# Kernel optimization log

Measured on AMD Instinct MI355X. Metric: run time of the kernel, lower is better.

The kernel has to match this reference:

```python
import jax, jax.numpy as jnp
import numpy as np

B, LATENT, HID, OUT, SEQ = 256, 512, 1024, 256, 128


def setup_inputs() -> dict:
    key = jax.random.key(0)
    ks = jax.random.split(key, 5)
    s = lambda fan: 1.0 / np.sqrt(fan)
    return {
        "latent": jax.random.normal(ks[0], (B, LATENT), jnp.float32),
        "fc_W": jax.random.normal(ks[1], (HID, LATENT), jnp.float32) * s(LATENT),
        "fc_b": jnp.zeros((HID,), jnp.float32),
        "W_ih": jax.random.normal(ks[2], (4 * HID, OUT), jnp.float32) * s(HID),
        "W_hh": jax.random.normal(ks[3], (4 * HID, HID), jnp.float32) * s(HID),
        "b_ih": jnp.zeros((4 * HID,), jnp.float32),
        "b_hh": jnp.zeros((4 * HID,), jnp.float32),
        "out_W": jax.random.normal(ks[4], (OUT, HID), jnp.float32) * s(HID),
        "out_b": jnp.zeros((OUT,), jnp.float32),
    }


def reference(latent, fc_W, fc_b, W_ih, W_hh, b_ih, b_hh, out_W, out_b):
    # hidden init from latent; cell init zero (num_layers = 1)
    h0 = latent @ fc_W.T + fc_b                       # [B, HID]
    c0 = jnp.zeros_like(h0)
    x0 = jnp.zeros((latent.shape[0], out_W.shape[0]), latent.dtype)  # [B, OUT]
    bias = b_ih + b_hh
    H = h0.shape[-1]

    def step(carry, _):
        x, h, c = carry
        gates = x @ W_ih.T + h @ W_hh.T + bias        # [B, 4H], torch order i,f,g,o
        i = jax.nn.sigmoid(gates[:, 0 * H:1 * H])
        f = jax.nn.sigmoid(gates[:, 1 * H:2 * H])
        g = jnp.tanh(gates[:, 2 * H:3 * H])
        o = jax.nn.sigmoid(gates[:, 3 * H:4 * H])
        c = f * c + i * g
        h = o * jnp.tanh(c)
        y = h @ out_W.T + out_b                        # [B, OUT]; fed back as next input
        return (y, h, c), y

    _, ys = jax.lax.scan(step, (x0, h0, c0), None, length=SEQ)
    return jnp.transpose(ys, (1, 0, 2))               # [B, SEQ, OUT]
```

## Files before the change

kernel.cpp:

```cpp
#include <hip/hip_runtime.h>


typedef __attribute__((ext_vector_type(8))) _Float16 f16x8;
typedef __attribute__((ext_vector_type(4))) float f32x4;
typedef __attribute__((ext_vector_type(4))) unsigned u32x4;

#define MFMA16(a,b,c) __builtin_amdgcn_mfma_f32_16x16x32_f16(a,b,c,0,0,0)

__device__ __forceinline__ short f2h(float x){
  return __builtin_bit_cast(short, (_Float16)x);
}
__device__ __forceinline__ unsigned pack2h(float a, float b){
  unsigned short ua = __builtin_bit_cast(unsigned short, (_Float16)a);
  unsigned short ub = __builtin_bit_cast(unsigned short, (_Float16)b);
  return (unsigned)ua | ((unsigned)ub << 16);
}

__device__ __forceinline__ void gll16(const void* g, void* l){
  __builtin_amdgcn_global_load_lds((const __attribute__((address_space(1))) void*)g,
                                   (__attribute__((address_space(3))) void*)l, 16, 0, 0);
}

__device__ __forceinline__ void vm0(){ asm volatile("s_waitcnt vmcnt(0)" ::: "memory"); }

__device__ __forceinline__ void stage_t(const short* gRC, int ldk, short* lds, int lane, int wv){
#pragma unroll
  for (int jj = 0; jj < 2; ++jj){
    int j = wv*2 + jj;
    const short* src = gRC + (size_t)(j*8 + (lane>>3))*ldk + ((lane&7)*8);
    gll16(src, lds + j*512);
  }
}

__device__ __forceinline__ f16x8 fragh(const short* t, int r, int kk, int lane){
  int row = r + (lane & 15);
  int k0  = (kk<<5) + ((lane>>4)<<3);
  return *(const f16x8*)(t + row*64 + (k0 ^ ((row & 7)<<3)));
}

template<int CH>
__device__ __forceinline__ void core_k(const short* Ag, const short* Bg, int ldk,
                                       short* As, short* Bs, f32x4 (&acc)[2][2],
                                       int lane, int wv, int wr, int wc){
  stage_t(Ag, ldk, As, lane, wv);
  stage_t(Bg, ldk, Bs, lane, wv);
  __syncthreads();
  int buf = 0;
  for (int c = 0; c < CH; ++c){
    if (c+1 < CH){
      stage_t(Ag + (c+1)*64, ldk, As + (buf^1)*4096, lane, wv);
      stage_t(Bg + (c+1)*64, ldk, Bs + (buf^1)*4096, lane, wv);
    }
    const short* At = As + buf*4096;
    const short* Bt = Bs + buf*4096;
#pragma unroll
    for (int kk = 0; kk < 2; ++kk){
      f16x8 a0 = fragh(At, wr,    kk, lane), a1 = fragh(At, wr+16, kk, lane);
      f16x8 b0 = fragh(Bt, wc,    kk, lane), b1 = fragh(Bt, wc+16, kk, lane);
      acc[0][0] = MFMA16(a0,b0,acc[0][0]); acc[0][1] = MFMA16(a0,b1,acc[0][1]);
      acc[1][0] = MFMA16(a1,b0,acc[1][0]); acc[1][1] = MFMA16(a1,b1,acc[1][1]);
    }
    __syncthreads();
    buf ^= 1;
  }
}


__global__ void k_prep(const float* __restrict__ W_ih, const float* __restrict__ out_W,
                       const float* __restrict__ latent, const float* __restrict__ fc_W,
                       const float* __restrict__ W_hh,
                       const float* __restrict__ b_ih, const float* __restrict__ b_hh,
                       short* __restrict__ WihF, short* __restrict__ owT,
                       short* __restrict__ owB, short* __restrict__ latF,
                       short* __restrict__ fcwF, short* __restrict__ W0F,
                       float* __restrict__ bias0, unsigned* __restrict__ flags){
  int T = blockDim.x*gridDim.x, t0 = blockIdx.x*blockDim.x + threadIdx.x;
  for (int i = t0; i < 8192; i += T) flags[i] = 0u;
  for (int idx = t0; idx < 4096*256; idx += T){
    int r = idx >> 8, j = idx & 255;
    WihF[(size_t)r*256 + (j ^ ((r&7)<<3))] = f2h(W_ih[idx]);
  }
  for (int idx = t0; idx < 1024*256; idx += T){
    int c = idx >> 8, j = idx & 255;
    owT[(size_t)c*256 + (j ^ ((c&7)<<3))] = f2h(out_W[(size_t)j*1024 + c]);
  }
  for (int idx = t0; idx < 256*1024; idx += T){
    int o = idx >> 10, k = idx & 1023;
    owB[(size_t)o*1024 + (k ^ ((o&7)<<3))] = f2h(out_W[idx]);
  }
  for (int idx = t0; idx < 256*512; idx += T){
    int b = idx >> 9, j = idx & 511;
    latF[(size_t)b*512 + (j ^ ((b&7)<<3))] = f2h(latent[idx]);
  }
  for (int idx = t0; idx < 1024*512; idx += T){
    int n = idx >> 9, j = idx & 511;
    fcwF[(size_t)n*512 + (j ^ ((n&7)<<3))] = f2h(fc_W[idx]);
  }
  for (int idx = t0; idx < 4096*1024; idx += T){
    int r = idx >> 10, k = idx & 1023;
    int p = ((r & 1023)<<2) | (r >> 10);
    size_t a = ((size_t)(p>>4)*32 + (k>>5))*512 + ((size_t)((((k>>3)&3)<<4)|(p&15)))*8 + (k&7);
    W0F[a] = f2h(W_hh[idx]);
  }
  for (int r = t0; r < 4096; r += T){
    int rp = ((r & 1023)<<2) | (r >> 10);
    bias0[rp] = b_ih[r] + b_hh[r];
  }
}

__global__ void k_bias1(const float* __restrict__ W_ih, const float* __restrict__ out_b,
                        const float* __restrict__ bias0, float* __restrict__ bias1){
  int r = blockIdx.x*256 + threadIdx.x;
  float s = 0.f;
  for (int j = 0; j < 256; ++j) s += W_ih[(size_t)r*256 + j]*out_b[j];
  int rp = ((r & 1023)<<2) | (r >> 10);
  bias1[rp] = bias0[rp] + s;
}

__global__ __launch_bounds__(256) void k_wtotal(const short* __restrict__ WihF,
                                                const short* __restrict__ owT,
                                                const float* __restrict__ W_hh,
                                                short* __restrict__ WtF){
  __shared__ __align__(16) short As[2*4096];
  __shared__ __align__(16) short Bs[2*4096];
  int tid = threadIdx.x, lane = tid & 63, wv = tid >> 6;
  int wr = (wv>>1)*32, wc = (wv&1)*32;
  int Rm = blockIdx.x*64, Rn = blockIdx.y*64;
  f32x4 acc[2][2] = {};
  core_k<4>(WihF + (size_t)Rm*256, owT + (size_t)Rn*256, 256, As, Bs, acc, lane, wv, wr, wc);
#pragma unroll
  for (int mi = 0; mi < 2; ++mi)
#pragma unroll
  for (int ni = 0; ni < 2; ++ni)
#pragma unroll
  for (int r = 0; r < 4; ++r){
    int row = Rm + wr + mi*16 + ((lane>>4)<<2) + r;
    int col = Rn + wc + ni*16 + (lane & 15);
    float v = acc[mi][ni][r] + W_hh[(size_t)row*1024 + col];
    int p = ((row & 1023)<<2) | (row >> 10);
    size_t a = ((size_t)(p>>4)*32 + (col>>5))*512 + ((size_t)((((col>>3)&3)<<4)|(p&15)))*8 + (col&7);
    WtF[a] = f2h(v);
  }
}

__global__ __launch_bounds__(256) void k_h0(const short* __restrict__ latF,
                                            const short* __restrict__ fcwF,
                                            const float* __restrict__ fc_b,
                                            short* __restrict__ A0){
  __shared__ __align__(16) short As[2*4096];
  __shared__ __align__(16) short Bs[2*4096];
  int tid = threadIdx.x, lane = tid & 63, wv = tid >> 6;
  int wr = (wv>>1)*32, wc = (wv&1)*32;
  int Rm = blockIdx.x*64, Rn = blockIdx.y*64;
  f32x4 acc[2][2] = {};
  core_k<8>(latF + (size_t)Rm*512, fcwF + (size_t)Rn*512, 512, As, Bs, acc, lane, wv, wr, wc);
#pragma unroll
  for (int mi = 0; mi < 2; ++mi)
#pragma unroll
  for (int ni = 0; ni < 2; ++ni)
#pragma unroll
  for (int r = 0; r < 4; ++r){
    int row = Rm + wr + mi*16 + ((lane>>4)<<2) + r;
    int col = Rn + wc + ni*16 + (lane & 15);
    float h = acc[mi][ni][r] + fc_b[col];
    A0[(size_t)row*1024 + (col ^ ((row&7)<<3))] = f2h(h);
  }
}

__global__ __launch_bounds__(512, 1) void k_persist(
    const short* __restrict__ WtF, const short* __restrict__ W0F,
    const float* __restrict__ bias0, const float* __restrict__ bias1,
    const short* __restrict__ A0, short* __restrict__ Hh,
    unsigned* __restrict__ flags){
  __shared__ __align__(16) short Asl[32*1024];
  __shared__ __align__(16) float Lg0[32*132];
  __shared__ __align__(16) float Lg1[32*132];
  const int tid = threadIdx.x, lane = tid & 63, wv = tid >> 6;
  const int wg = blockIdx.x;
  const int chain = wg & 7, gw = wg >> 3;
  const int wn = wv & 3, kh = wv >> 2;
  const int cbase = gw*8 + wn*2, sbase = kh*16;

  __builtin_amdgcn_fence(__ATOMIC_ACQUIRE, "agent");

  u32x4 braw[2][16];
  {
    const short* src = WtF + ((size_t)cbase*32 + sbase)*512 + lane*8;
#pragma unroll
    for (int cf = 0; cf < 2; ++cf)
#pragma unroll
      for (int s = 0; s < 16; ++s){
        const short* p = src + (size_t)(cf*32 + s)*512;
        asm volatile("global_load_dwordx4 %0, %1, off" : "=v"(braw[cf][s]) : "v"(p));
      }
    vm0();
  }
  const short* W0base = W0F + ((size_t)cbase*32 + sbase)*512 + lane*8;

  const int r0 = lane & 15;
  const int kql = (lane>>4)<<3;
  const int sw = (r0 & 7) << 3;

  const int er = tid >> 4, up = tid & 15;
  const int grow = chain*32 + er;
  const int swE = (grow & 7) << 3;
  const int posE = (gw*32 + 2*up) ^ swE;
  const f32x4 b1qA = *(const f32x4*)(bias1 + gw*128 + 8*up);
  const f32x4 b1qB = *(const f32x4*)(bias1 + gw*128 + 8*up + 4);
  float cA = 0.f, cB = 0.f;

  unsigned* flagC = flags + (size_t)chain*64;

  for (int t = 0; t < 128; ++t){
    {
      const short* base = (t == 0) ? A0 : (Hh + (size_t)(t-1)*262144);
      const short* bb = base + (size_t)(chain*32)*1024;
#pragma unroll
      for (int q = 0; q < 8; ++q){
        int i = wv*8 + q;
        gll16(bb + (size_t)(i>>1)*1024 + (i&1)*512 + lane*8, Asl + i*512);
      }
    }
    __syncthreads();

    f32x4 acc[2][2] = {};
    const short* Ar0 = Asl + r0*1024;
    const short* Ar1 = Asl + (16 + r0)*1024;
    if (t == 0){
#pragma unroll
      for (int s = 0; s < 16; ++s){
        int k = (sbase + s)*32 + kql;
        f16x8 w0 = *(const f16x8*)(W0base + (size_t)(0*32 + s)*512);
        f16x8 w1 = *(const f16x8*)(W0base + (size_t)(1*32 + s)*512);
        f16x8 a0 = *(const f16x8*)(Ar0 + (k ^ sw));
        f16x8 a1 = *(const f16x8*)(Ar1 + (k ^ sw));
        acc[0][0] = MFMA16(a0, w0, acc[0][0]);
        acc[0][1] = MFMA16(a0, w1, acc[0][1]);
        acc[1][0] = MFMA16(a1, w0, acc[1][0]);
        acc[1][1] = MFMA16(a1, w1, acc[1][1]);
      }
    } else {
#pragma unroll
      for (int s = 0; s < 16; ++s){
        int k = (sbase + s)*32 + kql;
        f16x8 a0 = *(const f16x8*)(Ar0 + (k ^ sw));
        f16x8 a1 = *(const f16x8*)(Ar1 + (k ^ sw));
        acc[0][0] = MFMA16(a0, __builtin_bit_cast(f16x8, braw[0][s]), acc[0][0]);
        acc[0][1] = MFMA16(a0, __builtin_bit_cast(f16x8, braw[1][s]), acc[0][1]);
        acc[1][0] = MFMA16(a1, __builtin_bit_cast(f16x8, braw[0][s]), acc[1][0]);
        acc[1][1] = MFMA16(a1, __builtin_bit_cast(f16x8, braw[1][s]), acc[1][1]);
      }
    }
    {
      float* Lg = kh ? Lg1 : Lg0;
#pragma unroll
      for (int rf = 0; rf < 2; ++rf)
#pragma unroll
      for (int cf = 0; cf < 2; ++cf)
#pragma unroll
      for (int j = 0; j < 4; ++j)
        Lg[(rf*16 + ((lane>>4)<<2) + j)*132 + wn*32 + cf*16 + r0] = acc[rf][cf][j];
    }
    __syncthreads();
    {
      f32x4 gA = *(const f32x4*)(Lg0 + er*132 + 8*up);
      f32x4 gB = *(const f32x4*)(Lg0 + er*132 + 8*up + 4);
      f32x4 hA = *(const f32x4*)(Lg1 + er*132 + 8*up);
      f32x4 hB = *(const f32x4*)(Lg1 + er*132 + 8*up + 4);
      if (t){ gA = gA + hA + b1qA; gB = gB + hB + b1qB; }
      else {
        gA = gA + hA + *(const f32x4*)(bias0 + gw*128 + 8*up);
        gB = gB + hB + *(const f32x4*)(bias0 + gw*128 + 8*up + 4);
      }
      float I0 = 1.f/(1.f+__expf(-gA[0])), F0 = 1.f/(1.f+__expf(-gA[1]));
      float G0 = tanhf(gA[2]),             O0 = 1.f/(1.f+__expf(-gA[3]));
      float I1 = 1.f/(1.f+__expf(-gB[0])), F1 = 1.f/(1.f+__expf(-gB[1]));
      float G1 = tanhf(gB[2]),             O1 = 1.f/(1.f+__expf(-gB[3]));
      cA = F0*cA + I0*G0;  float h0v = O0*tanhf(cA);
      cB = F1*cB + I1*G1;  float h1v = O1*tanhf(cB);
      unsigned pk = pack2h(h0v, h1v);
      short* pa = Hh + (size_t)t*262144 + (size_t)grow*1024 + posE;
      asm volatile("global_store_dword %0, %1, off sc0 sc1" :: "v"(pa), "v"(pk));
      vm0();
    }
    if (t < 127){
      __syncthreads();
      if (tid == 0){
        unsigned val = (unsigned)(t+1);
        unsigned* fp = flagC + gw;
        asm volatile("global_store_dword %0, %1, off sc0 sc1" :: "v"(fp), "v"(val) : "memory");
      }
      if (wv == 0){
        const unsigned* pp = flagC + (size_t)lane*4;
        unsigned tgt = (unsigned)(t+1);
        while (true){
          u32x4 f;
          asm volatile("global_load_dwordx4 %0, %1, off sc0 sc1\n\ts_waitcnt vmcnt(0)"
                       : "=v"(f) : "v"(pp) : "memory");
          bool ok = (lane >= 8) || (f[0] >= tgt && f[1] >= tgt && f[2] >= tgt && f[3] >= tgt);
          if (__all(ok)) break;
        }
      }
      __syncthreads();
    }
  }
}

__global__ __launch_bounds__(512) void k_y(const short* __restrict__ Hh,
                                           const short* __restrict__ owB,
                                           const float* __restrict__ out_b,
                                           float* __restrict__ out){
  __shared__ __align__(16) short As[2*8192];
  __shared__ __align__(16) short Bs[2*16384];
  int tid = threadIdx.x, lane = tid & 63, wv = tid >> 6;
  int wr = (wv>>2)*64, wc = (wv&3)*64;
  size_t Rm = (size_t)blockIdx.x * 128;
  const short* Ab = Hh + Rm*1024;
  f32x4 acc[4][4] = {};
  auto stA = [&](int c, short* dst){
#pragma unroll
    for (int jj = 0; jj < 2; ++jj){ int j = wv*2 + jj;
      gll16(Ab + (size_t)(j*8 + (lane>>3))*1024 + c*64 + (lane&7)*8, dst + j*512); }
  };
  auto stB = [&](int c, short* dst){
#pragma unroll
    for (int jj = 0; jj < 4; ++jj){ int j = wv*4 + jj;
      gll16(owB + (size_t)(j*8 + (lane>>3))*1024 + c*64 + (lane&7)*8, dst + j*512); }
  };
  stA(0, As); stB(0, Bs);
  __syncthreads();
  int buf = 0;
  for (int c = 0; c < 16; ++c){
    if (c+1 < 16){ stA(c+1, As + (buf^1)*8192); stB(c+1, Bs + (buf^1)*16384); }
    const short* At = As + buf*8192;
    const short* Bt = Bs + buf*16384;
#pragma unroll
    for (int kk = 0; kk < 2; ++kk){
      f16x8 av[4], bv[4];
#pragma unroll
      for (int mi = 0; mi < 4; ++mi) av[mi] = fragh(At, wr + mi*16, kk, lane);
#pragma unroll
      for (int ni = 0; ni < 4; ++ni) bv[ni] = fragh(Bt, wc + ni*16, kk, lane);
#pragma unroll
      for (int mi = 0; mi < 4; ++mi)
#pragma unroll
      for (int ni = 0; ni < 4; ++ni) acc[mi][ni] = MFMA16(av[mi], bv[ni], acc[mi][ni]);
    }
    __syncthreads();
    buf ^= 1;
  }
#pragma unroll
  for (int ni = 0; ni < 4; ++ni){
    int col = wc + ni*16 + (lane & 15);
    float bv = out_b[col];
#pragma unroll
    for (int mi = 0; mi < 4; ++mi)
#pragma unroll
    for (int r = 0; r < 4; ++r){
      size_t m = Rm + wr + mi*16 + ((lane>>4)<<2) + r;
      int t = (int)(m >> 8), bb = (int)(m & 255);
      out[(size_t)bb*32768 + (size_t)t*256 + col] = acc[mi][ni][r] + bv;
    }
  }
}

extern "C" void kernel_launch(void* const* d_in, const int* in_sizes, int n_in,
                              void* d_out, int out_size, void* d_ws, size_t ws_size,
                              hipStream_t stream) {
  (void)in_sizes; (void)n_in; (void)out_size; (void)ws_size;
  const float* latent = (const float*)d_in[0];
  const float* fc_W   = (const float*)d_in[1];
  const float* fc_b   = (const float*)d_in[2];
  const float* W_ih   = (const float*)d_in[3];
  const float* W_hh   = (const float*)d_in[4];
  const float* b_ih   = (const float*)d_in[5];
  const float* b_hh   = (const float*)d_in[6];
  const float* out_W  = (const float*)d_in[7];
  const float* out_b  = (const float*)d_in[8];
  float* out = (float*)d_out;
  char*  ws  = (char*)d_ws;
  const size_t MB = 1u << 20;
  short* WtF   = (short*)(ws + 0);
  short* W0F   = (short*)(ws + 8*MB);
  short* A0    = (short*)(ws + 16*MB);
  float* bias0 = (float*)(ws + 17*MB);
  float* bias1 = (float*)(ws + 17*MB + 65536);
  short* owB   = (short*)(ws + 17*MB + 131072);
  short* WihF  = (short*)(ws + 18*MB);
  short* owT   = (short*)(ws + 20*MB);
  short* latF  = (short*)(ws + 20*MB + 524288);
  short* fcwF  = (short*)(ws + 21*MB);
  unsigned* flg= (unsigned*)(ws + 22*MB);
  short* Hh    = (short*)(ws + 23*MB);

  k_prep<<<1024, 256, 0, stream>>>(W_ih, out_W, latent, fc_W, W_hh, b_ih, b_hh,
                                   WihF, owT, owB, latF, fcwF, W0F, bias0, flg);
  k_bias1<<<16, 256, 0, stream>>>(W_ih, out_b, bias0, bias1);
  k_wtotal<<<dim3(64,16), 256, 0, stream>>>(WihF, owT, W_hh, WtF);
  k_h0<<<dim3(4,16), 256, 0, stream>>>(latF, fcwF, fc_b, A0);
  k_persist<<<256, 512, 0, stream>>>(WtF, W0F, bias0, bias1, A0, Hh, flg);
  k_y<<<256, 512, 0, stream>>>(Hh, owB, out_b, out);
}
```

Measured before the change: 656.9 us.

## Split persistent LSTM batch chains into 16-row slices with two workgroups per CU

Each persistent workgroup now handles 16 batch rows instead of 32. This doubles the grid to 512 workgroups and raises launch bounds to 2 per CU. The work per step per wave is halved to one row-fragment of MFMAs, and only half the threads run the gate and cell update. The goal is to cut per-step latency on the serial recurrence by spreading rows across more co-resident workgroups. In exchange it needs more flag-synchronized chains, and it relies on all 512 workgroups being co-resident, so register and LDS pressure at two workgroups per CU could cause a deadlock or spills.

```diff
diff --git a/kernel.cpp b/kernel.cpp
--- a/kernel.cpp
+++ b/kernel.cpp
@@ -167,33 +167,30 @@
   }
 }
 
-__global__ __launch_bounds__(512, 1) void k_persist(
+__global__ __launch_bounds__(512, 2) void k_persist(
     const short* __restrict__ WtF, const short* __restrict__ W0F,
     const float* __restrict__ bias0, const float* __restrict__ bias1,
     const short* __restrict__ A0, short* __restrict__ Hh,
     unsigned* __restrict__ flags){
-  __shared__ __align__(16) short Asl[32*1024];
-  __shared__ __align__(16) float Lg0[32*132];
-  __shared__ __align__(16) float Lg1[32*132];
+  __shared__ __align__(16) short Asl[16*1024];
+  __shared__ __align__(16) float Lg0[16*132];
+  __shared__ __align__(16) float Lg1[16*132];
   const int tid = threadIdx.x, lane = tid & 63, wv = tid >> 6;
   const int wg = blockIdx.x;
-  const int chain = wg & 7, gw = wg >> 3;
+  const int chain = wg >> 5, gw = wg & 31;
   const int wn = wv & 3, kh = wv >> 2;
   const int cbase = gw*8 + wn*2, sbase = kh*16;
 
   __builtin_amdgcn_fence(__ATOMIC_ACQUIRE, "agent");
 
-  u32x4 braw[2][16];
+  f16x8 Breg[2][16];
   {
     const short* src = WtF + ((size_t)cbase*32 + sbase)*512 + lane*8;
 #pragma unroll
     for (int cf = 0; cf < 2; ++cf)
 #pragma unroll
-      for (int s = 0; s < 16; ++s){
-        const short* p = src + (size_t)(cf*32 + s)*512;
-        asm volatile("global_load_dwordx4 %0, %1, off" : "=v"(braw[cf][s]) : "v"(p));
-      }
-    vm0();
+      for (int s = 0; s < 16; ++s)
+        Breg[cf][s] = *(const f16x8*)(src + (size_t)(cf*32 + s)*512);
   }
   const short* W0base = W0F + ((size_t)cbase*32 + sbase)*512 + lane*8;
 
@@ -202,7 +199,7 @@
   const int sw = (r0 & 7) << 3;
 
   const int er = tid >> 4, up = tid & 15;
-  const int grow = chain*32 + er;
+  const int grow = chain*16 + (er & 15);
   const int swE = (grow & 7) << 3;
   const int posE = (gw*32 + 2*up) ^ swE;
   const f32x4 b1qA = *(const f32x4*)(bias1 + gw*128 + 8*up);
@@ -214,18 +211,17 @@
   for (int t = 0; t < 128; ++t){
     {
       const short* base = (t == 0) ? A0 : (Hh + (size_t)(t-1)*262144);
-      const short* bb = base + (size_t)(chain*32)*1024;
-#pragma unroll
-      for (int q = 0; q < 8; ++q){
-        int i = wv*8 + q;
+      const short* bb = base + (size_t)(chain*16)*1024;
+#pragma unroll
+      for (int q = 0; q < 4; ++q){
+        int i = wv*4 + q;
         gll16(bb + (size_t)(i>>1)*1024 + (i&1)*512 + lane*8, Asl + i*512);
       }
     }
     __syncthreads();
 
-    f32x4 acc[2][2] = {};
+    f32x4 acc[2] = {};
     const short* Ar0 = Asl + r0*1024;
-    const short* Ar1 = Asl + (16 + r0)*1024;
     if (t == 0){
 #pragma unroll
       for (int s = 0; s < 16; ++s){
@@ -233,36 +229,28 @@
         f16x8 w0 = *(const f16x8*)(W0base + (size_t)(0*32 + s)*512);
         f16x8 w1 = *(const f16x8*)(W0base + (size_t)(1*32 + s)*512);
         f16x8 a0 = *(const f16x8*)(Ar0 + (k ^ sw));
-        f16x8 a1 = *(const f16x8*)(Ar1 + (k ^ sw));
-        acc[0][0] = MFMA16(a0, w0, acc[0][0]);
-        acc[0][1] = MFMA16(a0, w1, acc[0][1]);
-        acc[1][0] = MFMA16(a1, w0, acc[1][0]);
-        acc[1][1] = MFMA16(a1, w1, acc[1][1]);
+        acc[0] = MFMA16(a0, w0, acc[0]);
+        acc[1] = MFMA16(a0, w1, acc[1]);
       }
     } else {
 #pragma unroll
       for (int s = 0; s < 16; ++s){
         int k = (sbase + s)*32 + kql;
         f16x8 a0 = *(const f16x8*)(Ar0 + (k ^ sw));
-        f16x8 a1 = *(const f16x8*)(Ar1 + (k ^ sw));
-        acc[0][0] = MFMA16(a0, __builtin_bit_cast(f16x8, braw[0][s]), acc[0][0]);
-        acc[0][1] = MFMA16(a0, __builtin_bit_cast(f16x8, braw[1][s]), acc[0][1]);
-        acc[1][0] = MFMA16(a1, __builtin_bit_cast(f16x8, braw[0][s]), acc[1][0]);
-        acc[1][1] = MFMA16(a1, __builtin_bit_cast(f16x8, braw[1][s]), acc[1][1]);
+        acc[0] = MFMA16(a0, Breg[0][s], acc[0]);
+        acc[1] = MFMA16(a0, Breg[1][s], acc[1]);
       }
     }
     {
       float* Lg = kh ? Lg1 : Lg0;
 #pragma unroll
-      for (int rf = 0; rf < 2; ++rf)
-#pragma unroll
       for (int cf = 0; cf < 2; ++cf)
 #pragma unroll
       for (int j = 0; j < 4; ++j)
-        Lg[(rf*16 + ((lane>>4)<<2) + j)*132 + wn*32 + cf*16 + r0] = acc[rf][cf][j];
+        Lg[(((lane>>4)<<2) + j)*132 + wn*32 + cf*16 + r0] = acc[cf][j];
     }
     __syncthreads();
-    {
+    if (tid < 256){
       f32x4 gA = *(const f32x4*)(Lg0 + er*132 + 8*up);
       f32x4 gB = *(const f32x4*)(Lg0 + er*132 + 8*up + 4);
       f32x4 hA = *(const f32x4*)(Lg1 + er*132 + 8*up);
@@ -281,8 +269,8 @@
       unsigned pk = pack2h(h0v, h1v);
       short* pa = Hh + (size_t)t*262144 + (size_t)grow*1024 + posE;
       asm volatile("global_store_dword %0, %1, off sc0 sc1" :: "v"(pa), "v"(pk));
-      vm0();
-    }
+    }
+    vm0();
     if (t < 127){
       __syncthreads();
       if (tid == 0){
@@ -398,6 +386,6 @@
   k_bias1<<<16, 256, 0, stream>>>(W_ih, out_b, bias0, bias1);
   k_wtotal<<<dim3(64,16), 256, 0, stream>>>(WihF, owT, W_hh, WtF);
   k_h0<<<dim3(4,16), 256, 0, stream>>>(latF, fcwF, fc_b, A0);
-  k_persist<<<256, 512, 0, stream>>>(WtF, W0F, bias0, bias1, A0, Hh, flg);
+  k_persist<<<512, 512, 0, stream>>>(WtF, W0F, bias0, bias1, A0, Hh, flg);
   k_y<<<256, 512, 0, stream>>>(Hh, owB, out_b, out);
 }
```

After: 1.213 ms. +84.7%, slower.
